# Kernel tuning notes

Measured on AMD Instinct MI355X. Metric: run time of the kernel, lower is better.

The kernel has to match this reference:

```python
import jax, jax.numpy as jnp
import numpy as np

D = 1024
B, S = 4, 2048

def setup_inputs() -> dict:
    key = jax.random.key(0)
    ks = jax.random.split(key, 9)
    scale = 1.0 / np.sqrt(D)
    return {
        "queries": jax.random.normal(ks[0], (B, S, D), dtype=jnp.float32),
        "keys": jax.random.normal(ks[1], (B, S, D), dtype=jnp.float32),
        "values": jax.random.normal(ks[2], (B, S, D), dtype=jnp.float32),
        # torch nn.Linear weights: [out, in], y = x @ W.T + b
        "Wq": jax.random.uniform(ks[3], (D, D), jnp.float32, -scale, scale),
        "bq": jax.random.uniform(ks[4], (D,), jnp.float32, -scale, scale),
        "Wk": jax.random.uniform(ks[5], (D, D), jnp.float32, -scale, scale),
        "bk": jax.random.uniform(ks[6], (D,), jnp.float32, -scale, scale),
        "Wv": jax.random.uniform(ks[7], (D, D), jnp.float32, -scale, scale),
        "bv": jax.random.uniform(ks[8], (D,), jnp.float32, -scale, scale),
    }

def reference(queries, keys, values, Wq, bq, Wk, bk, Wv, bv):
    # Linear projections (torch convention: x @ W.T + b)
    Q = jnp.einsum('bsd,ed->bse', queries, Wq) + bq  # [B,S,D]
    K = jnp.einsum('bsd,ed->bse', keys, Wk) + bk
    V = jnp.einsum('bsd,ed->bse', values, Wv) + bv
    # relu attention: no softmax, no scaling (faithful to source)
    scores = jax.nn.relu(jnp.einsum('bqd,bkd->bqk', Q, K))  # [B,S,S]
    return jnp.einsum('bqk,bkd->bqd', scores, V)
```

## Files before the change

kernel.cpp:

```cpp
#include <hip/hip_runtime.h>
#include <hip/hip_bf16.h>
#include <stdint.h>

typedef __bf16 bf16_t;
typedef __bf16 bf16x8 __attribute__((ext_vector_type(8)));
typedef float f32x16 __attribute__((ext_vector_type(16)));

#define TILE 128
#define BK 64

__device__ __forceinline__ void async_copy16(const bf16_t* g, bf16_t* l) {
    __builtin_amdgcn_global_load_lds(
        (const __attribute__((address_space(1))) unsigned int*)(uintptr_t)g,
        (__attribute__((address_space(3))) unsigned int*)(uintptr_t)l,
        16, 0, 0);
}

template<bool OUT_F32, bool RELU, int BIAS_MODE>
__global__ __launch_bounds__(256, 4)
void gemm_bt(const bf16_t* __restrict__ A, const bf16_t* __restrict__ B,
             const float* __restrict__ bias, void* __restrict__ Cp,
             int K, int ldc, long sAb, long sBb, long sCb)
{
    __shared__ bf16_t As[TILE * BK];
    __shared__ bf16_t Bs[TILE * BK];

    const int b  = blockIdx.z;
    const int nb = gridDim.x, mb = gridDim.y;
    const int SW = 4;
    int bid   = blockIdx.y * nb + blockIdx.x;
    int strip = bid / (mb * SW);
    int rem   = bid - strip * (mb * SW);
    int bm    = rem / SW;
    int bn    = strip * SW + (rem - bm * SW);
    const int blockM = bm * TILE;
    const int blockN = bn * TILE;

    const int t    = threadIdx.x;
    const int lane = t & 63;
    const int wave = t >> 6;
    const int wm   = (wave >> 1) * 64;
    const int wn   = (wave & 1) * 64;
    const int r32  = lane & 31;
    const int half = lane >> 5;
    const int kx   = r32 & 7;

    f32x16 acc[2][2] = {};

    const bf16_t* Ab = A + sAb * (long)b;
    const bf16_t* Bb = B + sBb * (long)b;

    const bf16_t* gA[4]; const bf16_t* gB[4];
    bf16_t* lA[4]; bf16_t* lB[4];
    #pragma unroll
    for (int j = 0; j < 4; j++) {
        int c   = t + j * 256;
        int row = c >> 3;
        int kcl = (c & 7) ^ (row & 7);
        gA[j] = Ab + (long)(blockM + row) * K + kcl * 8;
        gB[j] = Bb + (long)(blockN + row) * K + kcl * 8;
        lA[j] = &As[c * 8];
        lB[j] = &Bs[c * 8];
    }

    for (int k0 = 0; k0 < K; k0 += BK) {
        #pragma unroll
        for (int j = 0; j < 4; j++) async_copy16(gA[j] + k0, lA[j]);
        #pragma unroll
        for (int j = 0; j < 4; j++) async_copy16(gB[j] + k0, lB[j]);
        __syncthreads();

        #pragma unroll
        for (int ks = 0; ks < 4; ks++) {
            const int kc = ks * 2 + half;
            bf16x8 af[2], bfr[2];
            #pragma unroll
            for (int i = 0; i < 2; i++) {
                int R = wm + i * 32 + r32;
                af[i] = *(const bf16x8*)&As[(R * 8 + (kc ^ kx)) * 8];
            }
            #pragma unroll
            for (int j = 0; j < 2; j++) {
                int C = wn + j * 32 + r32;
                bfr[j] = *(const bf16x8*)&Bs[(C * 8 + (kc ^ kx)) * 8];
            }
            #pragma unroll
            for (int i = 0; i < 2; i++)
                #pragma unroll
                for (int j = 0; j < 2; j++)
                    acc[i][j] = __builtin_amdgcn_mfma_f32_32x32x16_bf16(
                                    af[i], bfr[j], acc[i][j], 0, 0, 0);
        }
        __syncthreads();
    }

    float*  Cf = (float*) Cp + sCb * (long)b;
    bf16_t* Ch = (bf16_t*)Cp + sCb * (long)b;
    #pragma unroll
    for (int ti = 0; ti < 2; ti++) {
        #pragma unroll
        for (int tj = 0; tj < 2; tj++) {
            const int gcol = blockN + wn + tj * 32 + r32;
            float bc = 0.f;
            if (BIAS_MODE == 1) bc = bias[gcol];
            #pragma unroll
            for (int reg = 0; reg < 16; reg++) {
                const int grow = blockM + wm + ti * 32
                               + (reg & 3) + 8 * (reg >> 2) + 4 * half;
                float vv = acc[ti][tj][reg];
                if (BIAS_MODE == 1) vv += bc;
                if (BIAS_MODE == 2) vv += bias[grow];
                if (RELU) vv = fmaxf(vv, 0.f);
                if (OUT_F32) Cf[(long)grow * ldc + gcol] = vv;
                else         Ch[(long)grow * ldc + gcol] = (bf16_t)vv;
            }
        }
    }
}

__global__ __launch_bounds__(256)
void cast_all_kernel(const float* __restrict__ q, const float* __restrict__ k,
                     const float* __restrict__ v, const float* __restrict__ Wq,
                     const float* __restrict__ Wk, const float* __restrict__ Wv,
                     bf16_t* __restrict__ ws)
{
    const long BIG = 1048576;
    const long SMALL = 131072;
    long id = (long)blockIdx.x * blockDim.x + threadIdx.x;
    const float* src; bf16_t* dst;
    if (id < 3 * BIG) {
        int s = (int)(id / BIG);
        long off = (id - (long)s * BIG) * 8;
        src = (s == 0 ? q : s == 1 ? k : v) + off;
        dst = ws + (long)s * 8388608 + off;
    } else {
        long id2 = id - 3 * BIG;
        int s = (int)(id2 / SMALL);
        long off = (id2 - (long)s * SMALL) * 8;
        src = (s == 0 ? Wq : s == 1 ? Wk : Wv) + off;
        dst = ws + 25165824L + (long)s * 1048576 + off;
    }
    float4 v0 = ((const float4*)src)[0];
    float4 v1 = ((const float4*)src)[1];
    alignas(16) bf16_t o[8];
    o[0]=(bf16_t)v0.x; o[1]=(bf16_t)v0.y; o[2]=(bf16_t)v0.z; o[3]=(bf16_t)v0.w;
    o[4]=(bf16_t)v1.x; o[5]=(bf16_t)v1.y; o[6]=(bf16_t)v1.z; o[7]=(bf16_t)v1.w;
    *(uint4*)dst = *(const uint4*)o;
}

extern "C" void kernel_launch(void* const* d_in, const int* in_sizes, int n_in,
                              void* d_out, int out_size, void* d_ws, size_t ws_size,
                              hipStream_t stream)
{
    const float* q   = (const float*)d_in[0];
    const float* k   = (const float*)d_in[1];
    const float* v   = (const float*)d_in[2];
    const float* Wq  = (const float*)d_in[3];
    const float* bq  = (const float*)d_in[4];
    const float* Wk  = (const float*)d_in[5];
    const float* bk  = (const float*)d_in[6];
    const float* Wv  = (const float*)d_in[7];
    const float* bv  = (const float*)d_in[8];

    const int B = 4, S = 2048, D = 1024;
    const int BS = B * S;

    bf16_t* ws  = (bf16_t*)d_ws;
    bf16_t* qb  = ws;
    bf16_t* kb  = ws + 8388608L;
    bf16_t* vb  = ws + 16777216L;
    bf16_t* Wqb = ws + 25165824L;
    bf16_t* Wkb = ws + 26214400L;
    bf16_t* Wvb = ws + 27262976L;
    bf16_t* Qp  = ws + 28311552L;
    bf16_t* Kp  = ws + 36700160L;
    bf16_t* VpT = ws + 45088768L;
    bf16_t* Sc  = ws;

    dim3 blk(256);

    cast_all_kernel<<<dim3(13824), blk, 0, stream>>>(q, k, v, Wq, Wk, Wv, ws);

    gemm_bt<false, false, 1><<<dim3(D / TILE, BS / TILE, 1), blk, 0, stream>>>(
        qb, Wqb, bq, Qp, D, D, 0L, 0L, 0L);

    gemm_bt<false, false, 1><<<dim3(D / TILE, BS / TILE, 1), blk, 0, stream>>>(
        kb, Wkb, bk, Kp, D, D, 0L, 0L, 0L);

    gemm_bt<false, false, 2><<<dim3(S / TILE, D / TILE, B), blk, 0, stream>>>(
        Wvb, vb, bv, VpT, D, S, 0L, (long)S * D, (long)D * S);

    gemm_bt<false, true, 0><<<dim3(S / TILE, S / TILE, B), blk, 0, stream>>>(
        Qp, Kp, nullptr, Sc, D, S, (long)S * D, (long)S * D, (long)S * S);

    gemm_bt<true, false, 0><<<dim3(D / TILE, S / TILE, B), blk, 0, stream>>>(
        Sc, VpT, nullptr, d_out, S, D, (long)S * S, (long)D * S, (long)S * D);
}
```

Measured before the change: 308.6 us.

## Fuse fp32-to-bf16 activation casts into projection GEMM tile loads

Removes the separate activation cast pass: the Q/K/V projection GEMMs now load fp32 activations directly, convert to bf16 in registers and store to LDS. Only the weights are still pre-cast. This drops a large read/write pass and shrinks the workspace, but the fp32 tiles are loaded synchronously instead of via async global-to-LDS copies and are re-read per column block with double the bytes. The tile swizzle width is also widened from 4 to 8.

```diff
diff --git a/kernel.cpp b/kernel.cpp
--- a/kernel.cpp
+++ b/kernel.cpp
@@ -16,9 +16,18 @@
         16, 0, 0);
 }
 
-template<bool OUT_F32, bool RELU, int BIAS_MODE>
+__device__ __forceinline__ void swizzle_tiles(int bid, int mbT, int& bm, int& bn)
+{
+    const int SW = 8;
+    int strip = bid / (mbT * SW);
+    int rem   = bid - strip * (mbT * SW);
+    bm = rem / SW;
+    bn = strip * SW + (rem - bm * SW);
+}
+
+template<int AF32, int BF32, bool OUT_F32, bool RELU, int BIAS_MODE>
 __global__ __launch_bounds__(256, 4)
-void gemm_bt(const bf16_t* __restrict__ A, const bf16_t* __restrict__ B,
+void gemm_bt(const void* __restrict__ Ap, const void* __restrict__ Bp,
              const float* __restrict__ bias, void* __restrict__ Cp,
              int K, int ldc, long sAb, long sBb, long sCb)
 {
@@ -26,13 +35,8 @@
     __shared__ bf16_t Bs[TILE * BK];
 
     const int b  = blockIdx.z;
-    const int nb = gridDim.x, mb = gridDim.y;
-    const int SW = 4;
-    int bid   = blockIdx.y * nb + blockIdx.x;
-    int strip = bid / (mb * SW);
-    int rem   = bid - strip * (mb * SW);
-    int bm    = rem / SW;
-    int bn    = strip * SW + (rem - bm * SW);
+    int bm, bn;
+    swizzle_tiles(blockIdx.y * gridDim.x + blockIdx.x, gridDim.y, bm, bn);
     const int blockM = bm * TILE;
     const int blockN = bn * TILE;
 
@@ -47,27 +51,58 @@
 
     f32x16 acc[2][2] = {};
 
-    const bf16_t* Ab = A + sAb * (long)b;
-    const bf16_t* Bb = B + sBb * (long)b;
-
-    const bf16_t* gA[4]; const bf16_t* gB[4];
+    const bf16_t* Abh = (const bf16_t*)Ap + sAb * (long)b;
+    const float*  Abf = (const float*) Ap + sAb * (long)b;
+    const bf16_t* Bbh = (const bf16_t*)Bp + sBb * (long)b;
+    const float*  Bbf = (const float*) Bp + sBb * (long)b;
+
+    const bf16_t* gAh[4]; const float* gAf[4];
+    const bf16_t* gBh[4]; const float* gBf[4];
     bf16_t* lA[4]; bf16_t* lB[4];
     #pragma unroll
     for (int j = 0; j < 4; j++) {
         int c   = t + j * 256;
         int row = c >> 3;
         int kcl = (c & 7) ^ (row & 7);
-        gA[j] = Ab + (long)(blockM + row) * K + kcl * 8;
-        gB[j] = Bb + (long)(blockN + row) * K + kcl * 8;
+        long ao = (long)(blockM + row) * K + kcl * 8;
+        long bo = (long)(blockN + row) * K + kcl * 8;
+        gAh[j] = Abh + ao;  gAf[j] = Abf + ao;
+        gBh[j] = Bbh + bo;  gBf[j] = Bbf + bo;
         lA[j] = &As[c * 8];
         lB[j] = &Bs[c * 8];
     }
 
     for (int k0 = 0; k0 < K; k0 += BK) {
-        #pragma unroll
-        for (int j = 0; j < 4; j++) async_copy16(gA[j] + k0, lA[j]);
-        #pragma unroll
-        for (int j = 0; j < 4; j++) async_copy16(gB[j] + k0, lB[j]);
+        if (AF32) {
+            #pragma unroll
+            for (int j = 0; j < 4; j++) {
+                const float* p = gAf[j] + k0;
+                float4 u0 = ((const float4*)p)[0];
+                float4 u1 = ((const float4*)p)[1];
+                bf16x8 w;
+                w[0]=(bf16_t)u0.x; w[1]=(bf16_t)u0.y; w[2]=(bf16_t)u0.z; w[3]=(bf16_t)u0.w;
+                w[4]=(bf16_t)u1.x; w[5]=(bf16_t)u1.y; w[6]=(bf16_t)u1.z; w[7]=(bf16_t)u1.w;
+                *(bf16x8*)lA[j] = w;
+            }
+        } else {
+            #pragma unroll
+            for (int j = 0; j < 4; j++) async_copy16(gAh[j] + k0, lA[j]);
+        }
+        if (BF32) {
+            #pragma unroll
+            for (int j = 0; j < 4; j++) {
+                const float* p = gBf[j] + k0;
+                float4 u0 = ((const float4*)p)[0];
+                float4 u1 = ((const float4*)p)[1];
+                bf16x8 w;
+                w[0]=(bf16_t)u0.x; w[1]=(bf16_t)u0.y; w[2]=(bf16_t)u0.z; w[3]=(bf16_t)u0.w;
+                w[4]=(bf16_t)u1.x; w[5]=(bf16_t)u1.y; w[6]=(bf16_t)u1.z; w[7]=(bf16_t)u1.w;
+                *(bf16x8*)lB[j] = w;
+            }
+        } else {
+            #pragma unroll
+            for (int j = 0; j < 4; j++) async_copy16(gBh[j] + k0, lB[j]);
+        }
         __syncthreads();
 
         #pragma unroll
@@ -119,27 +154,14 @@
 }
 
 __global__ __launch_bounds__(256)
-void cast_all_kernel(const float* __restrict__ q, const float* __restrict__ k,
-                     const float* __restrict__ v, const float* __restrict__ Wq,
-                     const float* __restrict__ Wk, const float* __restrict__ Wv,
-                     bf16_t* __restrict__ ws)
-{
-    const long BIG = 1048576;
-    const long SMALL = 131072;
+void cast_w_kernel(const float* __restrict__ Wq, const float* __restrict__ Wk,
+                   const float* __restrict__ Wv, bf16_t* __restrict__ ws)
+{
     long id = (long)blockIdx.x * blockDim.x + threadIdx.x;
-    const float* src; bf16_t* dst;
-    if (id < 3 * BIG) {
-        int s = (int)(id / BIG);
-        long off = (id - (long)s * BIG) * 8;
-        src = (s == 0 ? q : s == 1 ? k : v) + off;
-        dst = ws + (long)s * 8388608 + off;
-    } else {
-        long id2 = id - 3 * BIG;
-        int s = (int)(id2 / SMALL);
-        long off = (id2 - (long)s * SMALL) * 8;
-        src = (s == 0 ? Wq : s == 1 ? Wk : Wv) + off;
-        dst = ws + 25165824L + (long)s * 1048576 + off;
-    }
+    int s = (int)(id >> 17);
+    long off = (id & 131071) * 8;
+    const float* src = (s == 0 ? Wq : s == 1 ? Wk : Wv) + off;
+    bf16_t* dst = ws + (long)s * 1048576 + off;
     float4 v0 = ((const float4*)src)[0];
     float4 v1 = ((const float4*)src)[1];
     alignas(16) bf16_t o[8];
@@ -166,33 +188,30 @@
     const int BS = B * S;
 
     bf16_t* ws  = (bf16_t*)d_ws;
-    bf16_t* qb  = ws;
-    bf16_t* kb  = ws + 8388608L;
-    bf16_t* vb  = ws + 16777216L;
-    bf16_t* Wqb = ws + 25165824L;
-    bf16_t* Wkb = ws + 26214400L;
-    bf16_t* Wvb = ws + 27262976L;
-    bf16_t* Qp  = ws + 28311552L;
-    bf16_t* Kp  = ws + 36700160L;
-    bf16_t* VpT = ws + 45088768L;
-    bf16_t* Sc  = ws;
+    bf16_t* Wqb = ws;
+    bf16_t* Wkb = ws + 1048576L;
+    bf16_t* Wvb = ws + 2097152L;
+    bf16_t* Qp  = ws + 3145728L;
+    bf16_t* Kp  = ws + 11534336L;
+    bf16_t* VpT = ws + 19922944L;
+    bf16_t* Sc  = ws + 28311552L;
 
     dim3 blk(256);
 
-    cast_all_kernel<<<dim3(13824), blk, 0, stream>>>(q, k, v, Wq, Wk, Wv, ws);
-
-    gemm_bt<false, false, 1><<<dim3(D / TILE, BS / TILE, 1), blk, 0, stream>>>(
-        qb, Wqb, bq, Qp, D, D, 0L, 0L, 0L);
-
-    gemm_bt<false, false, 1><<<dim3(D / TILE, BS / TILE, 1), blk, 0, stream>>>(
-        kb, Wkb, bk, Kp, D, D, 0L, 0L, 0L);
-
-    gemm_bt<false, false, 2><<<dim3(S / TILE, D / TILE, B), blk, 0, stream>>>(
-        Wvb, vb, bv, VpT, D, S, 0L, (long)S * D, (long)D * S);
-
-    gemm_bt<false, true, 0><<<dim3(S / TILE, S / TILE, B), blk, 0, stream>>>(
+    cast_w_kernel<<<dim3(1536), blk, 0, stream>>>(Wq, Wk, Wv, ws);
+
+    gemm_bt<1, 0, false, false, 1><<<dim3(D / TILE, BS / TILE, 1), blk, 0, stream>>>(
+        q, Wqb, bq, Qp, D, D, 0L, 0L, 0L);
+
+    gemm_bt<1, 0, false, false, 1><<<dim3(D / TILE, BS / TILE, 1), blk, 0, stream>>>(
+        k, Wkb, bk, Kp, D, D, 0L, 0L, 0L);
+
+    gemm_bt<0, 1, false, false, 2><<<dim3(S / TILE, D / TILE, B), blk, 0, stream>>>(
+        Wvb, v, bv, VpT, D, S, 0L, (long)S * D, (long)D * S);
+
+    gemm_bt<0, 0, false, true, 0><<<dim3(S / TILE, S / TILE, B), blk, 0, stream>>>(
         Qp, Kp, nullptr, Sc, D, S, (long)S * D, (long)S * D, (long)S * S);
 
-    gemm_bt<true, false, 0><<<dim3(D / TILE, S / TILE, B), blk, 0, stream>>>(
+    gemm_bt<0, 0, true, false, 0><<<dim3(D / TILE, S / TILE, B), blk, 0, stream>>>(
         Sc, VpT, nullptr, d_out, S, D, (long)S * S, (long)D * S, (long)S * D);
 }
```

Result: slower. 370.1 us (+19.9%).
